# Performance work log

Measured on AMD Instinct MI355X. Metric: run time of the kernel, lower is better.

Reference implementation:

```python
import jax, jax.numpy as jnp
import numpy as np

B, C, H, W = 64, 3, 128, 128
P = 4                      # square patch (neib_shape)
NC = 512                   # num_cells
IN = C * P * P             # 48, lstm input_size
SY, SX = H // P, W // P    # 32, 32 grid steps


def setup_inputs() -> dict:
    key = jax.random.key(0)
    k1, k2, k3, k4, k5 = jax.random.split(key, 5)
    s = 1.0 / np.sqrt(NC)  # torch nn.LSTM init scale
    return {
        "batch": jax.random.normal(k1, (B, C, H, W), dtype=jnp.float32),
        "W_ih": jax.random.uniform(k2, (4 * NC, IN + NC), jnp.float32, -s, s),
        "W_hh": jax.random.uniform(k3, (4 * NC, NC), jnp.float32, -s, s),
        "b_ih": jax.random.uniform(k4, (4 * NC,), jnp.float32, -s, s),
        "b_hh": jax.random.uniform(k5, (4 * NC,), jnp.float32, -s, s),
    }


def _forward(batch, W_ih, W_hh, b_ih, b_hh):
    # Extract row-major patches: t = i*SX + j -> batch[:, :, i*P:(i+1)*P, j*P:(j+1)*P]
    # flattened in (C, P, P) order, matching LstmIterator.__get_item's reshape.
    x = batch.reshape(B, C, SY, P, SX, P)
    xs = x.transpose(2, 4, 0, 1, 3, 5).reshape(SY, SX, B, IN)  # (SY, SX, B, IN)

    bias = b_ih + b_hh

    def lstm_cell(h, c, inp):
        # torch gate order: i, f, g, o
        gates = inp @ W_ih.T + h @ W_hh.T + bias          # (B, 4*NC)
        i, f, g, o = jnp.split(gates, 4, axis=-1)
        c = jax.nn.sigmoid(f) * c + jax.nn.sigmoid(i) * jnp.tanh(g)
        h = jax.nn.sigmoid(o) * jnp.tanh(c)
        return h, c

    def col_step(hc, inputs):
        h, c = hc
        x_t, prev2 = inputs                               # prev2 = queue look-back (row above)
        h, c = lstm_cell(h, c, jnp.concatenate([x_t, prev2], axis=-1))
        return (h, c), h

    def row_step(carry, row_x):
        h, c, prev_row = carry                            # prev_row: (SX, B, NC)
        (h, c), row_out = jax.lax.scan(col_step, (h, c), (row_x, prev_row))
        return (h, c, row_out), row_out

    h0 = jnp.zeros((B, NC), jnp.float32)
    c0 = jnp.zeros((B, NC), jnp.float32)
    row0 = jnp.zeros((SX, B, NC), jnp.float32)            # queue yields zeros for first row
    _, outs = jax.lax.scan(row_step, (h0, c0, row0), xs)  # (SY, SX, B, NC)

    # to_image: cat -> (T,B,NC), permute -> (B,T,NC), reshape -> (B,NC,SY,SX)
    out = outs.reshape(SY * SX, B, NC).transpose(1, 0, 2).reshape(B, NC, SY, SX)
    return out


def reference(batch, W_ih, W_hh, b_ih, b_hh):
    return _forward(batch, W_ih, W_hh, b_ih, b_hh)
```

## Files before the change

kernel.cpp:

```cpp
#include <hip/hip_runtime.h>
#include <hip/hip_bf16.h>

#define TT   1024
#define KPAD 1088
#define LSTR 520

typedef __attribute__((ext_vector_type(8))) short short8;
typedef __attribute__((ext_vector_type(4))) float floatx4;
using bf16 = __hip_bfloat16;

__device__ __forceinline__ float frcp(float x) { return __builtin_amdgcn_rcpf(x); }
__device__ __forceinline__ float fsig(float x) { return frcp(1.f + __expf(-x)); }
__device__ __forceinline__ float ftanh(float x) {
    float e = __expf(2.f * fminf(fmaxf(x, -15.f), 15.f));
    return (e - 1.f) * frcp(e + 1.f);
}

__device__ __forceinline__ short8 sc_load16(const short* p) {
    short8 v;
    asm volatile("global_load_dwordx4 %0, %1, off sc0 sc1" : "=v"(v) : "v"(p) : "memory");
    return v;
}
__device__ __forceinline__ void wait_vm0() {
    asm volatile("s_waitcnt vmcnt(0)" ::: "memory");
    __builtin_amdgcn_sched_barrier(0);
}

__global__ void prep_wb(const float* __restrict__ Wih, const float* __restrict__ Whh,
                        const float* __restrict__ bih, const float* __restrict__ bhh,
                        bf16* __restrict__ Wc, float* __restrict__ bias) {
    int idx = blockIdx.x * 256 + threadIdx.x;
    int total = 2048 * KPAD;
    if (idx < total) {
        int row = idx / KPAD;
        int k = idx - row * KPAD;
        float v = 0.f;
        if (k < 48)       v = Wih[row * 560 + k];
        else if (k < 64)  v = 0.f;
        else if (k < 576) v = Wih[row * 560 + 48 + (k - 64)];
        else              v = Whh[row * 512 + (k - 576)];
        Wc[idx] = __float2bfloat16(v);
    }
    if (idx < 2048) bias[idx] = bih[idx] + bhh[idx];
}

__global__ void prep_x(const float* __restrict__ batch, bf16* __restrict__ xs) {
    int idx = blockIdx.x * 256 + threadIdx.x;
    int kk = idx & 63;
    int b  = (idx >> 6) & 63;
    int t  = idx >> 12;
    float v = 0.f;
    if (kk < 48) {
        int c = kk >> 4, py = (kk >> 2) & 3, px = kk & 3;
        int i = t >> 5, j = t & 31;
        v = batch[((b * 3 + c) * 128 + (i * 4 + py)) * 128 + (j * 4 + px)];
    }
    xs[idx] = __float2bfloat16(v);
}

__launch_bounds__(512, 1)
__global__ void lstm_persist(const bf16* __restrict__ Wc, const float* __restrict__ bias,
                             const bf16* __restrict__ xs, bf16* __restrict__ ring,
                             float* __restrict__ out, unsigned* __restrict__ flags)
{
    __shared__ float gsm[4][16][36];
    __shared__ short p2buf[2][16 * LSTR];
    __shared__ short hbuf[16 * LSTR];

    const int wg   = blockIdx.x;
    const int bg   = wg & 3;
    const int wgc  = wg >> 2;
    const int tid  = threadIdx.x;
    const int w    = tid >> 6;
    const int lane = tid & 63;
    const int mrow = lane & 15;
    const int quad = lane >> 4;
    const int gate = w & 3;
    const int sc   = w >> 2;

    const int grow = gate * 512 + wgc * 32 + sc * 16 + mrow;
    short8 wf[34];
    {
        const short* wsrc = (const short*)Wc + (size_t)grow * KPAD + quad * 8;
        #pragma unroll
        for (int i = 0; i < 34; ++i) wf[i] = *(const short8*)(wsrc + i * 32);
        #pragma unroll
        for (int i = 0; i < 34; ++i) { asm volatile("" : "+v"(wf[i])); }
    }
    const float bias_r = bias[grow];

    unsigned* gflags = flags + bg * 512;
    const short* ringS = (const short*)ring;

    const int r0 = 2 * w;
    floatx4 cst = {0.f, 0.f, 0.f, 0.f};

    {
        short8 z = {0, 0, 0, 0, 0, 0, 0, 0};
        *(short8*)&p2buf[0][(r0 + 0) * LSTR + lane * 8] = z;
        *(short8*)&p2buf[0][(r0 + 1) * LSTR + lane * 8] = z;
    }
    __syncthreads();

    for (int t = 0; t < TT; ++t) {
        short8 pv0, pv1;
        {
            const short* p2 = ringS + ((size_t)(((t + 1) & 63) * 64 + bg * 16 + r0)) * 512 + lane * 8;
            pv0 = sc_load16(p2);
            pv1 = sc_load16(p2 + 512);
        }

        floatx4 acc[4];
        #pragma unroll
        for (int r = 0; r < 4; ++r) acc[r] = (floatx4){0.f, 0.f, 0.f, 0.f};
        {
            const short* xrow = (const short*)xs + ((size_t)t * 64 + bg * 16 + mrow) * 64 + quad * 8;
            short8 xa0 = *(const short8*)(xrow);
            short8 xa1 = *(const short8*)(xrow + 32);
            acc[0] = __builtin_amdgcn_mfma_f32_16x16x32_bf16(xa0, wf[0], acc[0], 0, 0, 0);
            acc[1] = __builtin_amdgcn_mfma_f32_16x16x32_bf16(xa1, wf[1], acc[1], 0, 0, 0);
            const short* pb = &p2buf[t & 1][mrow * LSTR + quad * 8];
            #pragma unroll
            for (int i = 0; i < 16; ++i) {
                short8 a = *(const short8*)(pb + i * 32);
                acc[(2 + i) & 3] = __builtin_amdgcn_mfma_f32_16x16x32_bf16(a, wf[2 + i], acc[(2 + i) & 3], 0, 0, 0);
            }
        }

        if (t) {
            if (w == 7) {
                const unsigned tgt = (unsigned)t;
                unsigned v;
                do {
                    v = __hip_atomic_load(gflags + (lane & 31) * 16, __ATOMIC_RELAXED, __HIP_MEMORY_SCOPE_AGENT);
                } while (__any((int)(v < tgt)));
            }
            __syncthreads();
        }

        short8 hv0, hv1;
        {
            const short* hb = ringS + ((size_t)(((t + 31) & 63) * 64 + bg * 16 + r0)) * 512 + lane * 8;
            hv0 = sc_load16(hb);
            hv1 = sc_load16(hb + 512);
        }
        wait_vm0();
        *(short8*)&hbuf[(r0 + 0) * LSTR + lane * 8] = hv0;
        *(short8*)&hbuf[(r0 + 1) * LSTR + lane * 8] = hv1;
        {
            short* pd = &p2buf[(t + 1) & 1][0];
            *(short8*)&pd[(r0 + 0) * LSTR + lane * 8] = pv0;
            *(short8*)&pd[(r0 + 1) * LSTR + lane * 8] = pv1;
        }
        __syncthreads();

        {
            const short* hbp = &hbuf[mrow * LSTR + quad * 8];
            #pragma unroll
            for (int i = 0; i < 16; ++i) {
                short8 a = *(const short8*)(hbp + i * 32);
                acc[(18 + i) & 3] = __builtin_amdgcn_mfma_f32_16x16x32_bf16(a, wf[18 + i], acc[(18 + i) & 3], 0, 0, 0);
            }
        }
        floatx4 s = acc[0] + acc[1] + acc[2] + acc[3];
        #pragma unroll
        for (int r = 0; r < 4; ++r) gsm[gate][quad * 4 + r][sc * 16 + mrow] = s[r] + bias_r;
        __syncthreads();

        if (w < 2) {
            const int b16 = 8 * w + (lane >> 3);
            const int cj  = (lane & 7) * 4;
            floatx4 gi = *(const floatx4*)&gsm[0][b16][cj];
            floatx4 gf = *(const floatx4*)&gsm[1][b16][cj];
            floatx4 gg = *(const floatx4*)&gsm[2][b16][cj];
            floatx4 go = *(const floatx4*)&gsm[3][b16][cj];
            union { unsigned long long u; unsigned short sh[4]; } hp;
            floatx4 hh;
            #pragma unroll
            for (int k = 0; k < 4; ++k) {
                float c = fsig(gf[k]) * cst[k] + fsig(gi[k]) * ftanh(gg[k]);
                cst[k] = c;
                float h = fsig(go[k]) * ftanh(c);
                hh[k] = h;
                union { bf16 b; unsigned short u; } cv;
                cv.b = __float2bfloat16(h);
                hp.sh[k] = cv.u;
            }
            short* hst = (short*)ring + ((size_t)(((t + 32) & 63) * 64 + bg * 16 + b16)) * 512
                         + wgc * 32 + cj;
            __hip_atomic_store((unsigned long long*)hst, hp.u, __ATOMIC_RELAXED, __HIP_MEMORY_SCOPE_AGENT);
            asm volatile("s_waitcnt vmcnt(0)" ::: "memory");
            __builtin_amdgcn_sched_barrier(0);
            if (lane == 0)
                __hip_atomic_store(gflags + (wgc * 2 + w) * 16, (unsigned)(t + 1),
                                   __ATOMIC_RELAXED, __HIP_MEMORY_SCOPE_AGENT);
            *(floatx4*)(out + (size_t)(bg * 16 + b16) * TT * 512 + (size_t)t * 512 + wgc * 32 + cj) = hh;
        }
    }
}

extern "C" void kernel_launch(void* const* d_in, const int* in_sizes, int n_in,
                              void* d_out, int out_size, void* d_ws, size_t ws_size,
                              hipStream_t stream) {
    const float* batch = (const float*)d_in[0];
    const float* Wih   = (const float*)d_in[1];
    const float* Whh   = (const float*)d_in[2];
    const float* bih   = (const float*)d_in[3];
    const float* bhh   = (const float*)d_in[4];
    float* out = (float*)d_out;

    char* p = (char*)d_ws;
    bf16*  Wc     = (bf16*)p;     p += (size_t)2048 * KPAD * 2;
    float* bias   = (float*)p;    p += (size_t)2048 * 4;
    bf16*  xs     = (bf16*)p;     p += (size_t)TT * 64 * 64 * 2;
    bf16*  ring   = (bf16*)p;     p += (size_t)64 * 64 * 512 * 2;
    unsigned* flg = (unsigned*)p; p += 8192;

    hipMemsetAsync(ring, 0, (size_t)32 * 64 * 512 * 2, stream);
    hipMemsetAsync(flg, 0, 8192, stream);

    prep_wb<<<(2048 * KPAD + 255) / 256, 256, 0, stream>>>(Wih, Whh, bih, bhh, Wc, bias);
    prep_x<<<(TT * 64 * 64) / 256, 256, 0, stream>>>(batch, xs);

    lstm_persist<<<64, 512, 0, stream>>>(Wc, bias, xs, ring, out, flg);
}
```

Baseline: 2.902 ms.

## Replace flag-based barrier with tagged ring entries carrying step counters

Drops the separate per-group flag array and spin barrier. Each bf16 pair of h values is now stored alongside a 32-bit timestep tag in a 64-bit word, so consumers check the tags on the data they load and re-poll until they match, with no extra round trip to a flag array. This takes the flag poll, the extra syncthreads and the serialized store-wait-flag sequence off the per-step critical path. In exchange the ring traffic doubles, loads go from two to eight per step, and the ring shrinks to 48 slots with modular slot counters.

```diff
diff --git a/kernel.cpp b/kernel.cpp
--- a/kernel.cpp
+++ b/kernel.cpp
@@ -1,13 +1,16 @@
 #include <hip/hip_runtime.h>
 #include <hip/hip_bf16.h>
 
-#define TT   1024
-#define KPAD 1088
-#define LSTR 520
+#define TT    1024
+#define KPAD  1088
+#define LSTR  520
+#define NSLOT 48
 
 typedef __attribute__((ext_vector_type(8))) short short8;
 typedef __attribute__((ext_vector_type(4))) float floatx4;
+typedef __attribute__((ext_vector_type(4))) unsigned int uintx4;
 using bf16 = __hip_bfloat16;
+typedef unsigned long long ull;
 
 __device__ __forceinline__ float frcp(float x) { return __builtin_amdgcn_rcpf(x); }
 __device__ __forceinline__ float fsig(float x) { return frcp(1.f + __expf(-x)); }
@@ -16,8 +19,8 @@
     return (e - 1.f) * frcp(e + 1.f);
 }
 
-__device__ __forceinline__ short8 sc_load16(const short* p) {
-    short8 v;
+__device__ __forceinline__ uintx4 sc_load16u(const void* p) {
+    uintx4 v;
     asm volatile("global_load_dwordx4 %0, %1, off sc0 sc1" : "=v"(v) : "v"(p) : "memory");
     return v;
 }
@@ -61,7 +64,7 @@
 __launch_bounds__(512, 1)
 __global__ void lstm_persist(const bf16* __restrict__ Wc, const float* __restrict__ bias,
                              const bf16* __restrict__ xs, bf16* __restrict__ ring,
-                             float* __restrict__ out, unsigned* __restrict__ flags)
+                             float* __restrict__ out)
 {
     __shared__ float gsm[4][16][36];
     __shared__ short p2buf[2][16 * LSTR];
@@ -89,8 +92,7 @@
     }
     const float bias_r = bias[grow];
 
-    unsigned* gflags = flags + bg * 512;
-    const short* ringS = (const short*)ring;
+    char* ringB = (char*)ring;
 
     const int r0 = 2 * w;
     floatx4 cst = {0.f, 0.f, 0.f, 0.f};
@@ -102,13 +104,15 @@
     }
     __syncthreads();
 
+    int sl_h = 31, sl_p = 1, sl_w = 32;
+
     for (int t = 0; t < TT; ++t) {
-        short8 pv0, pv1;
-        {
-            const short* p2 = ringS + ((size_t)(((t + 1) & 63) * 64 + bg * 16 + r0)) * 512 + lane * 8;
-            pv0 = sc_load16(p2);
-            pv1 = sc_load16(p2 + 512);
-        }
+        const char* hgp = ringB + ((size_t)(sl_h * 64 + bg * 16 + r0)) * 2048 + lane * 32;
+        uintx4 a0 = sc_load16u(hgp),        a1 = sc_load16u(hgp + 16);
+        uintx4 a2 = sc_load16u(hgp + 2048), a3 = sc_load16u(hgp + 2064);
+        const char* pgp = ringB + ((size_t)(sl_p * 64 + bg * 16 + r0)) * 2048 + lane * 32;
+        uintx4 b0 = sc_load16u(pgp),        b1 = sc_load16u(pgp + 16);
+        uintx4 b2 = sc_load16u(pgp + 2048), b3 = sc_load16u(pgp + 2064);
 
         floatx4 acc[4];
         #pragma unroll
@@ -127,30 +131,40 @@
             }
         }
 
-        if (t) {
-            if (w == 7) {
-                const unsigned tgt = (unsigned)t;
-                unsigned v;
-                do {
-                    v = __hip_atomic_load(gflags + (lane & 31) * 16, __ATOMIC_RELAXED, __HIP_MEMORY_SCOPE_AGENT);
-                } while (__any((int)(v < tgt)));
-            }
-            __syncthreads();
-        }
-
-        short8 hv0, hv1;
-        {
-            const short* hb = ringS + ((size_t)(((t + 31) & 63) * 64 + bg * 16 + r0)) * 512 + lane * 8;
-            hv0 = sc_load16(hb);
-            hv1 = sc_load16(hb + 512);
-        }
         wait_vm0();
-        *(short8*)&hbuf[(r0 + 0) * LSTR + lane * 8] = hv0;
-        *(short8*)&hbuf[(r0 + 1) * LSTR + lane * 8] = hv1;
-        {
+        {
+            const unsigned expp = (t >= 31) ? (unsigned)(t - 30) : 0u;
+            for (;;) {
+                unsigned m = (b0.y ^ expp) | (b0.w ^ expp) | (b1.y ^ expp) | (b1.w ^ expp)
+                           | (b2.y ^ expp) | (b2.w ^ expp) | (b3.y ^ expp) | (b3.w ^ expp);
+                if (!__any((int)m)) break;
+                b0 = sc_load16u(pgp);        b1 = sc_load16u(pgp + 16);
+                b2 = sc_load16u(pgp + 2048); b3 = sc_load16u(pgp + 2064);
+                wait_vm0();
+            }
+        }
+        {
+            const unsigned exph = (unsigned)t;
+            for (;;) {
+                unsigned m = (a0.y ^ exph) | (a0.w ^ exph) | (a1.y ^ exph) | (a1.w ^ exph)
+                           | (a2.y ^ exph) | (a2.w ^ exph) | (a3.y ^ exph) | (a3.w ^ exph);
+                if (!__any((int)m)) break;
+                a0 = sc_load16u(hgp);        a1 = sc_load16u(hgp + 16);
+                a2 = sc_load16u(hgp + 2048); a3 = sc_load16u(hgp + 2064);
+                wait_vm0();
+            }
+        }
+
+        {
+            uintx4 h0 = {a0.x, a0.z, a1.x, a1.z};
+            uintx4 h1 = {a2.x, a2.z, a3.x, a3.z};
+            *(uintx4*)&hbuf[(r0 + 0) * LSTR + lane * 8] = h0;
+            *(uintx4*)&hbuf[(r0 + 1) * LSTR + lane * 8] = h1;
+            uintx4 p0 = {b0.x, b0.z, b1.x, b1.z};
+            uintx4 p1 = {b2.x, b2.z, b3.x, b3.z};
             short* pd = &p2buf[(t + 1) & 1][0];
-            *(short8*)&pd[(r0 + 0) * LSTR + lane * 8] = pv0;
-            *(short8*)&pd[(r0 + 1) * LSTR + lane * 8] = pv1;
+            *(uintx4*)&pd[(r0 + 0) * LSTR + lane * 8] = p0;
+            *(uintx4*)&pd[(r0 + 1) * LSTR + lane * 8] = p1;
         }
         __syncthreads();
 
@@ -174,8 +188,8 @@
             floatx4 gf = *(const floatx4*)&gsm[1][b16][cj];
             floatx4 gg = *(const floatx4*)&gsm[2][b16][cj];
             floatx4 go = *(const floatx4*)&gsm[3][b16][cj];
-            union { unsigned long long u; unsigned short sh[4]; } hp;
             floatx4 hh;
+            unsigned short hu[4];
             #pragma unroll
             for (int k = 0; k < 4; ++k) {
                 float c = fsig(gf[k]) * cst[k] + fsig(gi[k]) * ftanh(gg[k]);
@@ -184,18 +198,21 @@
                 hh[k] = h;
                 union { bf16 b; unsigned short u; } cv;
                 cv.b = __float2bfloat16(h);
-                hp.sh[k] = cv.u;
-            }
-            short* hst = (short*)ring + ((size_t)(((t + 32) & 63) * 64 + bg * 16 + b16)) * 512
-                         + wgc * 32 + cj;
-            __hip_atomic_store((unsigned long long*)hst, hp.u, __ATOMIC_RELAXED, __HIP_MEMORY_SCOPE_AGENT);
-            asm volatile("s_waitcnt vmcnt(0)" ::: "memory");
-            __builtin_amdgcn_sched_barrier(0);
-            if (lane == 0)
-                __hip_atomic_store(gflags + (wgc * 2 + w) * 16, (unsigned)(t + 1),
-                                   __ATOMIC_RELAXED, __HIP_MEMORY_SCOPE_AGENT);
+                hu[k] = cv.u;
+            }
+            unsigned d01 = (unsigned)hu[0] | ((unsigned)hu[1] << 16);
+            unsigned d23 = (unsigned)hu[2] | ((unsigned)hu[3] << 16);
+            ull tg = ((ull)(unsigned)(t + 1)) << 32;
+            ull* wp = (ull*)(ringB + ((size_t)(sl_w * 64 + bg * 16 + b16)) * 2048
+                             + ((size_t)(wgc * 16 + (lane & 7) * 2)) * 8);
+            __hip_atomic_store(wp,     (ull)d01 | tg, __ATOMIC_RELAXED, __HIP_MEMORY_SCOPE_AGENT);
+            __hip_atomic_store(wp + 1, (ull)d23 | tg, __ATOMIC_RELAXED, __HIP_MEMORY_SCOPE_AGENT);
             *(floatx4*)(out + (size_t)(bg * 16 + b16) * TT * 512 + (size_t)t * 512 + wgc * 32 + cj) = hh;
         }
+
+        sl_h = (sl_h + 1 == NSLOT) ? 0 : sl_h + 1;
+        sl_p = (sl_p + 1 == NSLOT) ? 0 : sl_p + 1;
+        sl_w = (sl_w + 1 == NSLOT) ? 0 : sl_w + 1;
     }
 }
 
@@ -213,14 +230,12 @@
     bf16*  Wc     = (bf16*)p;     p += (size_t)2048 * KPAD * 2;
     float* bias   = (float*)p;    p += (size_t)2048 * 4;
     bf16*  xs     = (bf16*)p;     p += (size_t)TT * 64 * 64 * 2;
-    bf16*  ring   = (bf16*)p;     p += (size_t)64 * 64 * 512 * 2;
-    unsigned* flg = (unsigned*)p; p += 8192;
-
-    hipMemsetAsync(ring, 0, (size_t)32 * 64 * 512 * 2, stream);
-    hipMemsetAsync(flg, 0, 8192, stream);
+    bf16*  ring   = (bf16*)p;     p += (size_t)NSLOT * 64 * 2048;
+
+    hipMemsetAsync(ring, 0, (size_t)32 * 64 * 2048, stream);
 
     prep_wb<<<(2048 * KPAD + 255) / 256, 256, 0, stream>>>(Wih, Whh, bih, bhh, Wc, bias);
     prep_x<<<(TT * 64 * 64) / 256, 256, 0, stream>>>(batch, xs);
 
-    lstm_persist<<<64, 512, 0, stream>>>(Wc, bias, xs, ring, out, flg);
-}
+    lstm_persist<<<64, 512, 0, stream>>>(Wc, bias, xs, ring, out);
+}
```

Measured after the change: 3.754 ms. +29.4%, slower.

## Halve workgroup to four waves, each owning two weight tiles, with pipelined flag polling

Applied to the files above, without the earlier changes.

The persistent LSTM kernel now runs 256 threads per workgroup instead of 512. Each wave holds two 16-row weight slices in registers (68 short8 fragments) and issues two MFMAs per LDS-loaded A fragment, which halves LDS reads per MFMA and halves the number of waves taking part in barriers. The input-projection MFMAs are moved after the flag wait so they overlap the h-ring loads. Flag polling keeps two loads in flight, and the flags are packed more densely (stride 2 instead of 16). This roughly doubles register pressure per lane and halves wave-level parallelism on the serial critical path, and the denser flags may share cache lines with concurrent writers.

```diff
diff --git a/kernel.cpp b/kernel.cpp
--- a/kernel.cpp
+++ b/kernel.cpp
@@ -58,7 +58,7 @@
     xs[idx] = __float2bfloat16(v);
 }
 
-__launch_bounds__(512, 1)
+__launch_bounds__(256, 1)
 __global__ void lstm_persist(const bf16* __restrict__ Wc, const float* __restrict__ bias,
                              const bf16* __restrict__ xs, bf16* __restrict__ ring,
                              float* __restrict__ out, unsigned* __restrict__ flags)
@@ -75,82 +75,109 @@
     const int lane = tid & 63;
     const int mrow = lane & 15;
     const int quad = lane >> 4;
-    const int gate = w & 3;
-    const int sc   = w >> 2;
-
-    const int grow = gate * 512 + wgc * 32 + sc * 16 + mrow;
-    short8 wf[34];
+
+    const int growA = w * 512 + wgc * 32 + mrow;
+    const int growB = growA + 16;
+    short8 wfA[34], wfB[34];
     {
-        const short* wsrc = (const short*)Wc + (size_t)grow * KPAD + quad * 8;
-        #pragma unroll
-        for (int i = 0; i < 34; ++i) wf[i] = *(const short8*)(wsrc + i * 32);
-        #pragma unroll
-        for (int i = 0; i < 34; ++i) { asm volatile("" : "+v"(wf[i])); }
-    }
-    const float bias_r = bias[grow];
-
-    unsigned* gflags = flags + bg * 512;
+        const short* wsA = (const short*)Wc + (size_t)growA * KPAD + quad * 8;
+        const short* wsB = (const short*)Wc + (size_t)growB * KPAD + quad * 8;
+        #pragma unroll
+        for (int i = 0; i < 34; ++i) { wfA[i] = *(const short8*)(wsA + i * 32);
+                                       wfB[i] = *(const short8*)(wsB + i * 32); }
+        #pragma unroll
+        for (int i = 0; i < 34; ++i) { asm volatile("" : "+v"(wfA[i]));
+                                       asm volatile("" : "+v"(wfB[i])); }
+    }
+    const float biasA = bias[growA];
+    const float biasB = bias[growB];
+
+    unsigned* gflags = flags + bg * 64;
     const short* ringS = (const short*)ring;
 
-    const int r0 = 2 * w;
+    const int r0 = 4 * w;
     floatx4 cst = {0.f, 0.f, 0.f, 0.f};
 
     {
         short8 z = {0, 0, 0, 0, 0, 0, 0, 0};
-        *(short8*)&p2buf[0][(r0 + 0) * LSTR + lane * 8] = z;
-        *(short8*)&p2buf[0][(r0 + 1) * LSTR + lane * 8] = z;
+        #pragma unroll
+        for (int j = 0; j < 4; ++j) *(short8*)&p2buf[0][(r0 + j) * LSTR + lane * 8] = z;
     }
     __syncthreads();
 
     for (int t = 0; t < TT; ++t) {
-        short8 pv0, pv1;
+        short8 pv0, pv1, pv2, pv3;
         {
             const short* p2 = ringS + ((size_t)(((t + 1) & 63) * 64 + bg * 16 + r0)) * 512 + lane * 8;
-            pv0 = sc_load16(p2);
-            pv1 = sc_load16(p2 + 512);
-        }
-
-        floatx4 acc[4];
-        #pragma unroll
-        for (int r = 0; r < 4; ++r) acc[r] = (floatx4){0.f, 0.f, 0.f, 0.f};
+            pv0 = sc_load16(p2);        pv1 = sc_load16(p2 + 512);
+            pv2 = sc_load16(p2 + 1024); pv3 = sc_load16(p2 + 1536);
+        }
+        short8 xa0, xa1;
         {
             const short* xrow = (const short*)xs + ((size_t)t * 64 + bg * 16 + mrow) * 64 + quad * 8;
-            short8 xa0 = *(const short8*)(xrow);
-            short8 xa1 = *(const short8*)(xrow + 32);
-            acc[0] = __builtin_amdgcn_mfma_f32_16x16x32_bf16(xa0, wf[0], acc[0], 0, 0, 0);
-            acc[1] = __builtin_amdgcn_mfma_f32_16x16x32_bf16(xa1, wf[1], acc[1], 0, 0, 0);
+            xa0 = *(const short8*)(xrow);
+            xa1 = *(const short8*)(xrow + 32);
+            asm volatile("" : "+v"(xa0), "+v"(xa1));
+        }
+
+        floatx4 accA[4], accB[4];
+        #pragma unroll
+        for (int r = 0; r < 4; ++r) { accA[r] = (floatx4){0.f, 0.f, 0.f, 0.f};
+                                      accB[r] = (floatx4){0.f, 0.f, 0.f, 0.f}; }
+        {
             const short* pb = &p2buf[t & 1][mrow * LSTR + quad * 8];
             #pragma unroll
             for (int i = 0; i < 16; ++i) {
                 short8 a = *(const short8*)(pb + i * 32);
-                acc[(2 + i) & 3] = __builtin_amdgcn_mfma_f32_16x16x32_bf16(a, wf[2 + i], acc[(2 + i) & 3], 0, 0, 0);
+                accA[(2 + i) & 3] = __builtin_amdgcn_mfma_f32_16x16x32_bf16(a, wfA[2 + i], accA[(2 + i) & 3], 0, 0, 0);
+                accB[(2 + i) & 3] = __builtin_amdgcn_mfma_f32_16x16x32_bf16(a, wfB[2 + i], accB[(2 + i) & 3], 0, 0, 0);
             }
         }
 
         if (t) {
-            if (w == 7) {
+            if (w == 3) {
                 const unsigned tgt = (unsigned)t;
-                unsigned v;
-                do {
-                    v = __hip_atomic_load(gflags + (lane & 31) * 16, __ATOMIC_RELAXED, __HIP_MEMORY_SCOPE_AGENT);
-                } while (__any((int)(v < tgt)));
+                const unsigned* fp = gflags + (lane & 31) * 2;
+                unsigned va, vb;
+                asm volatile("global_load_dword %0, %1, off sc0 sc1" : "=v"(va) : "v"(fp) : "memory");
+                asm volatile("global_load_dword %0, %1, off sc0 sc1" : "=v"(vb) : "v"(fp) : "memory");
+                for (;;) {
+                    asm volatile("s_waitcnt vmcnt(1)" ::: "memory");
+                    __builtin_amdgcn_sched_barrier(0);
+                    if (!__any((int)(va < tgt))) break;
+                    asm volatile("global_load_dword %0, %1, off sc0 sc1" : "=v"(va) : "v"(fp) : "memory");
+                    asm volatile("s_waitcnt vmcnt(1)" ::: "memory");
+                    __builtin_amdgcn_sched_barrier(0);
+                    if (!__any((int)(vb < tgt))) break;
+                    asm volatile("global_load_dword %0, %1, off sc0 sc1" : "=v"(vb) : "v"(fp) : "memory");
+                }
+                wait_vm0();
             }
             __syncthreads();
         }
 
-        short8 hv0, hv1;
+        short8 hv0, hv1, hv2, hv3;
         {
             const short* hb = ringS + ((size_t)(((t + 31) & 63) * 64 + bg * 16 + r0)) * 512 + lane * 8;
-            hv0 = sc_load16(hb);
-            hv1 = sc_load16(hb + 512);
-        }
+            hv0 = sc_load16(hb);        hv1 = sc_load16(hb + 512);
+            hv2 = sc_load16(hb + 1024); hv3 = sc_load16(hb + 1536);
+        }
+        accA[0] = __builtin_amdgcn_mfma_f32_16x16x32_bf16(xa0, wfA[0], accA[0], 0, 0, 0);
+        accA[1] = __builtin_amdgcn_mfma_f32_16x16x32_bf16(xa1, wfA[1], accA[1], 0, 0, 0);
+        accB[0] = __builtin_amdgcn_mfma_f32_16x16x32_bf16(xa0, wfB[0], accB[0], 0, 0, 0);
+        accB[1] = __builtin_amdgcn_mfma_f32_16x16x32_bf16(xa1, wfB[1], accB[1], 0, 0, 0);
+
         wait_vm0();
         *(short8*)&hbuf[(r0 + 0) * LSTR + lane * 8] = hv0;
         *(short8*)&hbuf[(r0 + 1) * LSTR + lane * 8] = hv1;
+        *(short8*)&hbuf[(r0 + 2) * LSTR + lane * 8] = hv2;
+        *(short8*)&hbuf[(r0 + 3) * LSTR + lane * 8] = hv3;
         {
             short* pd = &p2buf[(t + 1) & 1][0];
             *(short8*)&pd[(r0 + 0) * LSTR + lane * 8] = pv0;
             *(short8*)&pd[(r0 + 1) * LSTR + lane * 8] = pv1;
+            *(short8*)&pd[(r0 + 2) * LSTR + lane * 8] = pv2;
+            *(short8*)&pd[(r0 + 3) * LSTR + lane * 8] = pv3;
         }
         __syncthreads();
 
@@ -159,12 +186,19 @@
             #pragma unroll
             for (int i = 0; i < 16; ++i) {
                 short8 a = *(const short8*)(hbp + i * 32);
-                acc[(18 + i) & 3] = __builtin_amdgcn_mfma_f32_16x16x32_bf16(a, wf[18 + i], acc[(18 + i) & 3], 0, 0, 0);
-            }
-        }
-        floatx4 s = acc[0] + acc[1] + acc[2] + acc[3];
-        #pragma unroll
-        for (int r = 0; r < 4; ++r) gsm[gate][quad * 4 + r][sc * 16 + mrow] = s[r] + bias_r;
+                accA[(18 + i) & 3] = __builtin_amdgcn_mfma_f32_16x16x32_bf16(a, wfA[18 + i], accA[(18 + i) & 3], 0, 0, 0);
+                accB[(18 + i) & 3] = __builtin_amdgcn_mfma_f32_16x16x32_bf16(a, wfB[18 + i], accB[(18 + i) & 3], 0, 0, 0);
+            }
+        }
+        {
+            floatx4 sA = accA[0] + accA[1] + accA[2] + accA[3];
+            floatx4 sB = accB[0] + accB[1] + accB[2] + accB[3];
+            #pragma unroll
+            for (int r = 0; r < 4; ++r) {
+                gsm[w][quad * 4 + r][mrow]      = sA[r] + biasA;
+                gsm[w][quad * 4 + r][16 + mrow] = sB[r] + biasB;
+            }
+        }
         __syncthreads();
 
         if (w < 2) {
@@ -192,7 +226,7 @@
             asm volatile("s_waitcnt vmcnt(0)" ::: "memory");
             __builtin_amdgcn_sched_barrier(0);
             if (lane == 0)
-                __hip_atomic_store(gflags + (wgc * 2 + w) * 16, (unsigned)(t + 1),
+                __hip_atomic_store(gflags + (wgc * 2 + w) * 2, (unsigned)(t + 1),
                                    __ATOMIC_RELAXED, __HIP_MEMORY_SCOPE_AGENT);
             *(floatx4*)(out + (size_t)(bg * 16 + b16) * TT * 512 + (size_t)t * 512 + wgc * 32 + cj) = hh;
         }
@@ -214,13 +248,13 @@
     float* bias   = (float*)p;    p += (size_t)2048 * 4;
     bf16*  xs     = (bf16*)p;     p += (size_t)TT * 64 * 64 * 2;
     bf16*  ring   = (bf16*)p;     p += (size_t)64 * 64 * 512 * 2;
-    unsigned* flg = (unsigned*)p; p += 8192;
+    unsigned* flg = (unsigned*)p; p += 1024;
 
     hipMemsetAsync(ring, 0, (size_t)32 * 64 * 512 * 2, stream);
-    hipMemsetAsync(flg, 0, 8192, stream);
+    hipMemsetAsync(flg, 0, 1024, stream);
 
     prep_wb<<<(2048 * KPAD + 255) / 256, 256, 0, stream>>>(Wih, Whh, bih, bhh, Wc, bias);
     prep_x<<<(TT * 64 * 64) / 256, 256, 0, stream>>>(batch, xs);
 
-    lstm_persist<<<64, 512, 0, stream>>>(Wc, bias, xs, ring, out, flg);
-}
+    lstm_persist<<<64, 256, 0, stream>>>(Wc, bias, xs, ring, out, flg);
+}
```

Measured after the change: 3.272 ms. 1.13x slower.
